# Kernel optimization log

Hardware: AMD Instinct MI355X
Metric: run time of the kernel (lower is better)

The kernel has to match this reference:

```python
import jax, jax.numpy as jnp
import numpy as np

K = 10
NUM_BLKS = 6
LN_EPS = 1e-6
NODE_D = 64


def layer_norm(x, g, b):
    m = jnp.mean(x, axis=-1, keepdims=True)
    v = jnp.var(x, axis=-1, keepdims=True)
    return (x - m) * jax.lax.rsqrt(v + LN_EPS) * g + b


def setup_inputs() -> dict:
    key = jax.random.key(0)
    B, N_c, N_t, D_S, D_F = 4, 4096, 1024, 3, 4
    D_IN = 4 + D_S + D_F  # obs-embed(4) + s + f
    ks = jax.random.split(key, 32)
    sc = 0.02
    inp = {
        "s_ctx": jax.random.normal(ks[0], (B, N_c, D_S), jnp.float32),
        "f_ctx": jax.random.normal(ks[1], (B, N_c, D_F), jnp.float32),
        "s_test": jax.random.normal(ks[2], (B, N_t, D_S), jnp.float32),
        "valid_lens_ctx": jax.random.randint(ks[3], (B,), N_c // 2, N_c + 1).astype(jnp.int32),
        # embed_obs: nn.Embed(2, 4)
        "emb_obs": jax.random.normal(ks[4], (2, 4), jnp.float32) * sc,
        # embed_all: MLP([256,128,64], gelu)
        "ea_W0": jax.random.normal(ks[5], (D_IN, 256), jnp.float32) * sc, "ea_b0": jnp.zeros((256,), jnp.float32),
        "ea_W1": jax.random.normal(ks[6], (256, 128), jnp.float32) * sc, "ea_b1": jnp.zeros((128,), jnp.float32),
        "ea_W2": jax.random.normal(ks[7], (128, NODE_D), jnp.float32) * sc, "ea_b2": jnp.zeros((NODE_D,), jnp.float32),
        # top-level LayerNorm
        "ln_g": jnp.ones((NODE_D,), jnp.float32), "ln_b": jnp.zeros((NODE_D,), jnp.float32),
        # GraphKRBlock params, stacked over NUM_BLKS blocks
        "blk_Wm0": jax.random.normal(ks[8], (NUM_BLKS, NODE_D + 1, 128), jnp.float32) * sc,
        "blk_bm0": jnp.zeros((NUM_BLKS, 128), jnp.float32),
        "blk_Wm1": jax.random.normal(ks[9], (NUM_BLKS, 128, NODE_D), jnp.float32) * sc,
        "blk_bm1": jnp.zeros((NUM_BLKS, NODE_D), jnp.float32),
        "blk_Wu0": jax.random.normal(ks[10], (NUM_BLKS, 2 * NODE_D, 128), jnp.float32) * sc,
        "blk_bu0": jnp.zeros((NUM_BLKS, 128), jnp.float32),
        "blk_Wu1": jax.random.normal(ks[11], (NUM_BLKS, 128, NODE_D), jnp.float32) * sc,
        "blk_bu1": jnp.zeros((NUM_BLKS, NODE_D), jnp.float32),
        "blk_lng": jnp.ones((NUM_BLKS, NODE_D), jnp.float32),
        "blk_lnb": jnp.zeros((NUM_BLKS, NODE_D), jnp.float32),
        # head: MLP([256,64,2], gelu)
        "hd_W0": jax.random.normal(ks[12], (NODE_D, 256), jnp.float32) * sc, "hd_b0": jnp.zeros((256,), jnp.float32),
        "hd_W1": jax.random.normal(ks[13], (256, 64), jnp.float32) * sc, "hd_b1": jnp.zeros((64,), jnp.float32),
        "hd_W2": jax.random.normal(ks[14], (64, 2), jnp.float32) * sc, "hd_b2": jnp.zeros((2,), jnp.float32),
    }
    return inp


def reference(s_ctx, f_ctx, s_test, valid_lens_ctx,
              emb_obs, ea_W0, ea_b0, ea_W1, ea_b1, ea_W2, ea_b2, ln_g, ln_b,
              blk_Wm0, blk_bm0, blk_Wm1, blk_bm1, blk_Wu0, blk_bu0, blk_Wu1, blk_bu1,
              blk_lng, blk_lnb, hd_W0, hd_b0, hd_W1, hd_b1, hd_W2, hd_b2):
    B, N_c, _ = s_ctx.shape
    N_t = s_test.shape[1]

    # --- per-sample O(n^2) KNN graph build (custom_k_nearest_senders, l2 dist) ---
    mask = jnp.arange(N_c)[None, :] < valid_lens_ctx[:, None]          # [B,N_c]
    s_send = jnp.where(mask[..., None], s_ctx, 1e6)                    # invalid -> far away
    rx = jnp.concatenate([s_ctx, s_test], axis=1)                      # [B,N,d_s] receivers
    d = jnp.sqrt(jnp.sum((rx[:, :, None, :] - s_send[:, None, :, :]) ** 2, axis=-1))  # [B,N,N_c]
    negd, senders = jax.lax.top_k(-d, K)                               # k-nearest: [B,N,K]
    dists = -negd                                                       # ascending distances

    # --- embeddings: stack(embed_obs, s, f) -> embed_all MLP -> LayerNorm ---
    def embed(x):
        h = jax.nn.gelu(x @ ea_W0 + ea_b0)
        h = jax.nn.gelu(h @ ea_W1 + ea_b1)
        h = h @ ea_W2 + ea_b2
        return layer_norm(h, ln_g, ln_b)

    ctx_in = jnp.concatenate(
        [jnp.broadcast_to(emb_obs[1], (B, N_c, emb_obs.shape[1])), s_ctx, f_ctx], axis=-1)
    test_in = jnp.concatenate(
        [jnp.broadcast_to(emb_obs[0], (B, N_t, emb_obs.shape[1])), s_test,
         jnp.zeros((B, N_t, f_ctx.shape[-1]), f_ctx.dtype)], axis=-1)
    nodes = jnp.concatenate([embed(ctx_in), embed(test_in)], axis=1)   # [B,N,64]

    # --- num_blks GraphKRBlock message-passing blocks ---
    bidx = jnp.arange(B)[:, None, None]
    w = jax.nn.softmax(-dists, axis=-1)                                # kernel weights per receiver
    for i in range(NUM_BLKS):
        sf = nodes[bidx, senders]                                      # gather senders [B,N,K,64]
        m_in = jnp.concatenate([sf, dists[..., None]], axis=-1)        # [B,N,K,65]
        m = jax.nn.gelu(m_in @ blk_Wm0[i] + blk_bm0[i]) @ blk_Wm1[i] + blk_bm1[i]
        agg = jnp.einsum('bnk,bnkd->bnd', w, m)                        # scatter-to-receivers
        u_in = jnp.concatenate([nodes, agg], axis=-1)                  # [B,N,128]
        upd = jax.nn.gelu(u_in @ blk_Wu0[i] + blk_bu0[i]) @ blk_Wu1[i] + blk_bu1[i]
        nodes = layer_norm(nodes + upd, blk_lng[i], blk_lnb[i])

    # --- head on test nodes ---
    x_t = nodes[:, N_c:, :]                                            # [B,N_t,64]
    h = jax.nn.gelu(x_t @ hd_W0 + hd_b0)
    h = jax.nn.gelu(h @ hd_W1 + hd_b1)
    f_dist = h @ hd_W2 + hd_b2                                         # [B,N_t,2]
    f_mu, f_log_var = jnp.split(f_dist, 2, axis=-1)
    f_std = jnp.exp(f_log_var / 2)                                     # min_std = 0.0
    return f_mu, f_std
```

## Files before the change

kernel.cpp:

```cpp
#include <hip/hip_runtime.h>
#include <math.h>

#define BB 4
#define NC 4096
#define NT 1024
#define NN (NC + NT)
#define NODES (BB * NN)
#define DD 64
#define KNN 10
#define NBLK 6
#define BIGF 3.0e38f

typedef __attribute__((ext_vector_type(8))) short short8;
typedef __attribute__((ext_vector_type(4))) float f32x4;
typedef __attribute__((ext_vector_type(4))) int int4v;

__device__ __forceinline__ unsigned short f2bf(float f) {
    unsigned int u = __float_as_uint(f);
    unsigned int r = (u + 0x7fffu + ((u >> 16) & 1u)) >> 16;
    return (unsigned short)r;
}
__device__ __forceinline__ float bf2f(unsigned short h) {
    return __uint_as_float(((unsigned int)h) << 16);
}

__device__ __forceinline__ float gelu_f(float x) {
    const float c0 = 0.7978845608028654f;
    float x3 = x * x * x;
    float z2 = 2.0f * c0 * (x + 0.044715f * x3);
    float e = __expf(z2);
    float r = __builtin_amdgcn_rcpf(1.0f + e);
    return x - x * r;
}

__device__ __forceinline__ float wave_sum(float v) {
#pragma unroll
    for (int off = 32; off > 0; off >>= 1) v += __shfl_xor(v, off, 64);
    return v;
}

__device__ __forceinline__ f32x4 mfma_bf16(short8 a, short8 b, f32x4 c) {
    asm("v_mfma_f32_16x16x32_bf16 %0, %1, %2, %0" : "+v"(c) : "v"(a), "v"(b));
    return c;
}


__global__ __launch_bounds__(256) void k_convw(
    const float* __restrict__ Wm0, const float* __restrict__ Wm1,
    const float* __restrict__ Wu0, const float* __restrict__ Wu1,
    const float* __restrict__ bm0,
    const float* __restrict__ eW0, const float* __restrict__ eW1,
    const float* __restrict__ eW2,
    const float* __restrict__ hW0, const float* __restrict__ hW1,
    const float* __restrict__ sctx, const int* __restrict__ valid_lens,
    unsigned short* __restrict__ wtm0, unsigned short* __restrict__ wtm1p,
    unsigned short* __restrict__ wtu0, unsigned short* __restrict__ wtu1,
    float* __restrict__ wdp, float* __restrict__ bm0p,
    unsigned short* __restrict__ wte0, unsigned short* __restrict__ wte1,
    unsigned short* __restrict__ wte2,
    unsigned short* __restrict__ wth0, unsigned short* __restrict__ wth1,
    float4* __restrict__ s4)
{
    int t = blockIdx.x * 256 + threadIdx.x;
    if (t < 49152) {
        int i = t / 8192, r = t % 8192, n = r / 64, k = r % 64;
        wtm0[t] = f2bf(Wm0[(i * 65 + k) * 128 + n]);
    } else if (t < 98304) {
        int u = t - 49152;
        int i = u / 8192, r = u % 8192, n = r / 128, cp = r % 128;
        int col = ((cp & 7) << 4) | (cp >> 3);
        wtm1p[u] = f2bf(Wm1[(i * 128 + col) * 64 + n]);
    } else if (t < 196608) {
        int u = t - 98304;
        int i = u / 16384, r = u % 16384, n = r / 128, k = r % 128;
        wtu0[u] = f2bf(Wu0[(i * 128 + k) * 128 + n]);
    } else if (t < 245760) {
        int u = t - 196608;
        int i = u / 8192, r = u % 8192, n = r / 128, k = r % 128;
        wtu1[u] = f2bf(Wu1[(i * 128 + k) * 64 + n]);
    } else if (t < 246528) {
        int u = t - 245760;
        int i = u / 128, cp = u % 128;
        int col = ((cp & 7) << 4) | (cp >> 3);
        wdp[u] = Wm0[(i * 65 + 64) * 128 + col];
    } else if (t < 247296) {
        int u = t - 246528;
        int i = u / 128, cp = u % 128;
        int col = ((cp & 7) << 4) | (cp >> 3);
        bm0p[u] = bm0[i * 128 + col];
    } else if (t < 255488) {
        int u = t - 247296;
        int n = u / 32, k = u % 32;
        wte0[u] = (k < 11) ? f2bf(eW0[k * 256 + n]) : 0;
    } else if (t < 288256) {
        int u = t - 255488;
        int n = u / 256, k = u % 256;
        wte1[u] = f2bf(eW1[k * 128 + n]);
    } else if (t < 296448) {
        int u = t - 288256;
        int n = u / 128, k = u % 128;
        wte2[u] = f2bf(eW2[k * 64 + n]);
    } else if (t < 312832) {
        int u = t - 296448;
        int n = u / 64, k = u % 64;
        wth0[u] = f2bf(hW0[k * 256 + n]);
    } else if (t < 329216) {
        int u = t - 312832;
        int n = u / 256, k = u % 256;
        wth1[u] = f2bf(hW1[k * 64 + n]);
    } else if (t < 329216 + BB * NC) {
        int u = t - 329216;
        int b = u / NC, j = u % NC;
        bool ok = j < valid_lens[b];
        float x = ok ? sctx[u * 3] : 1.0e6f;
        float y = ok ? sctx[u * 3 + 1] : 1.0e6f;
        float z = ok ? sctx[u * 3 + 2] : 1.0e6f;
        s4[u] = make_float4(x, y, z, 0.0f);
    }
}

__global__ __launch_bounds__(256) void k_embed2(
    const float* __restrict__ s_ctx, const float* __restrict__ f_ctx,
    const float* __restrict__ s_test, const float* __restrict__ emb_obs,
    const unsigned short* __restrict__ WT0, const float* __restrict__ b0,
    const unsigned short* __restrict__ WT1, const float* __restrict__ b1,
    const unsigned short* __restrict__ WT2, const float* __restrict__ b2,
    const float* __restrict__ g, const float* __restrict__ bta,
    const unsigned short* __restrict__ Wm0n,
    unsigned short* __restrict__ nodes,
    unsigned short* __restrict__ Pout)
{
    __shared__ unsigned short H0[4][16 * 256];
    __shared__ unsigned short H1[4][16 * 128];
    __shared__ unsigned short XO[4][16 * 64];
    int t = threadIdx.x;
    int wave = t >> 6, lane = t & 63, lr = lane & 15, lk = lane >> 4;
    int rb = wave * 16;
    int n0 = blockIdx.x * 64;
    int bq = n0 / NN, nloc0 = n0 % NN;
    bool is_ctx = nloc0 < NC;
    int nr = nloc0 + rb + lr;
    float xv[8];
#pragma unroll
    for (int j = 0; j < 8; ++j) xv[j] = 0.0f;
    if (lk == 0) {
        const float* eb = emb_obs + (is_ctx ? 4 : 0);
        xv[0] = eb[0]; xv[1] = eb[1]; xv[2] = eb[2]; xv[3] = eb[3];
        if (is_ctx) {
            const float* sp = s_ctx + ((size_t)(bq * NC + nr)) * 3;
            const float* fp = f_ctx + ((size_t)(bq * NC + nr)) * 4;
            xv[4] = sp[0]; xv[5] = sp[1]; xv[6] = sp[2]; xv[7] = fp[0];
        } else {
            const float* sp = s_test + ((size_t)(bq * NT + nr - NC)) * 3;
            xv[4] = sp[0]; xv[5] = sp[1]; xv[6] = sp[2];
        }
    } else if (lk == 1 && is_ctx) {
        const float* fp = f_ctx + ((size_t)(bq * NC + nr)) * 4;
        xv[0] = fp[1]; xv[1] = fp[2]; xv[2] = fp[3];
    }
    short8 a;
#pragma unroll
    for (int j = 0; j < 8; ++j) a[j] = (short)f2bf(xv[j]);

    f32x4 acc0[16];
#pragma unroll
    for (int nt = 0; nt < 16; ++nt) {
        short8 bb = *(const short8*)(WT0 + (nt * 16 + lr) * 32 + lk * 8);
        f32x4 z = (f32x4){0.f, 0.f, 0.f, 0.f};
        acc0[nt] = mfma_bf16(a, bb, z);
    }
    unsigned short* h0 = &H0[wave][0];
#pragma unroll
    for (int nt = 0; nt < 16; ++nt) {
        int col = nt * 16 + lr;
        float bias = b0[col];
        int u = col >> 3;
#pragma unroll
        for (int j = 0; j < 4; ++j) {
            int row = lk * 4 + j;
            float v = gelu_f(acc0[nt][j] + bias);
            int us = (u & 16) | ((u ^ row) & 15);
            h0[row * 256 + us * 8 + (col & 7)] = f2bf(v);
        }
    }
    f32x4 acc1[8];
#pragma unroll
    for (int nt = 0; nt < 8; ++nt) acc1[nt] = (f32x4){0.f, 0.f, 0.f, 0.f};
#pragma unroll
    for (int ks = 0; ks < 8; ++ks) {
        int u = ks * 4 + lk;
        int us = (u & 16) | ((u ^ lr) & 15);
        short8 aa = *(const short8*)(&h0[lr * 256 + us * 8]);
#pragma unroll
        for (int nt = 0; nt < 8; ++nt) {
            short8 bb = *(const short8*)(WT1 + (nt * 16 + lr) * 256 + ks * 32 + lk * 8);
            acc1[nt] = mfma_bf16(aa, bb, acc1[nt]);
        }
    }
    unsigned short* h1 = &H1[wave][0];
#pragma unroll
    for (int nt = 0; nt < 8; ++nt) {
        int col = nt * 16 + lr;
        float bias = b1[col];
        int u = col >> 3;
#pragma unroll
        for (int j = 0; j < 4; ++j) {
            int row = lk * 4 + j;
            float v = gelu_f(acc1[nt][j] + bias);
            int us = (u ^ row) & 15;
            h1[row * 128 + us * 8 + (col & 7)] = f2bf(v);
        }
    }
    f32x4 acc2[4];
#pragma unroll
    for (int nt = 0; nt < 4; ++nt) acc2[nt] = (f32x4){0.f, 0.f, 0.f, 0.f};
#pragma unroll
    for (int ks = 0; ks < 4; ++ks) {
        int u = ks * 4 + lk;
        int us = (u ^ lr) & 15;
        short8 aa = *(const short8*)(&h1[lr * 128 + us * 8]);
#pragma unroll
        for (int nt = 0; nt < 4; ++nt) {
            short8 bb = *(const short8*)(WT2 + (nt * 16 + lr) * 128 + ks * 32 + lk * 8);
            acc2[nt] = mfma_bf16(aa, bb, acc2[nt]);
        }
    }
    float vals[4][4];
#pragma unroll
    for (int j = 0; j < 4; ++j)
#pragma unroll
        for (int nt = 0; nt < 4; ++nt)
            vals[j][nt] = acc2[nt][j] + b2[nt * 16 + lr];
    unsigned short* xo = &XO[wave][0];
#pragma unroll
    for (int j = 0; j < 4; ++j) {
        float s = vals[j][0] + vals[j][1] + vals[j][2] + vals[j][3];
#pragma unroll
        for (int m = 1; m < 16; m <<= 1) s += __shfl_xor(s, m, 64);
        float mean = s * (1.0f / 64.0f);
        float vs = 0.0f;
#pragma unroll
        for (int nt = 0; nt < 4; ++nt) { float d = vals[j][nt] - mean; vs += d * d; }
#pragma unroll
        for (int m = 1; m < 16; m <<= 1) vs += __shfl_xor(vs, m, 64);
        float inv = rsqrtf(vs * (1.0f / 64.0f) + 1e-6f);
        int row = lk * 4 + j;
        int node = n0 + rb + row;
#pragma unroll
        for (int nt = 0; nt < 4; ++nt) {
            int col = nt * 16 + lr;
            float o = (vals[j][nt] - mean) * inv * g[col] + bta[col];
            unsigned short ob = f2bf(o);
            nodes[(size_t)node * 64 + col] = ob;
            xo[row * 64 + ((col >> 3) ^ (row & 7)) * 8 + (col & 7)] = ob;
        }
    }
    f32x4 accP[8];
#pragma unroll
    for (int nt = 0; nt < 8; ++nt) accP[nt] = (f32x4){0.f, 0.f, 0.f, 0.f};
#pragma unroll
    for (int ks = 0; ks < 2; ++ks) {
        short8 aa = *(const short8*)(&xo[lr * 64 + ((ks * 4 + lk) ^ (lr & 7)) * 8]);
#pragma unroll
        for (int nt = 0; nt < 8; ++nt) {
            short8 bb = *(const short8*)(Wm0n + (nt * 16 + lr) * 64 + ks * 32 + lk * 8);
            accP[nt] = mfma_bf16(aa, bb, accP[nt]);
        }
    }
#pragma unroll
    for (int j = 0; j < 4; ++j) {
        int node = n0 + rb + lk * 4 + j;
        short8 ps;
#pragma unroll
        for (int nt = 0; nt < 8; ++nt) ps[nt] = (short)f2bf(accP[nt][j]);
        *(short8*)(Pout + (size_t)node * 128 + lr * 8) = ps;
    }
}

__global__ __launch_bounds__(256) void k_topk(
    const float4* __restrict__ s4, const float* __restrict__ s_ctx,
    const float* __restrict__ s_test,
    float* __restrict__ dists, int* __restrict__ senders, float* __restrict__ wout)
{
    __shared__ float cd[4 * 64 * 11];
    __shared__ float seld[4][4][12];
    __shared__ int   seli[4][4][12];
    __shared__ int   eqis[4][4][12];
    int wave = threadIdx.x >> 6;
    int lane = threadIdx.x & 63;
    int r0 = blockIdx.x * 16 + wave * 4;
    int b = r0 / NN;
    const float4* sc = s4 + (size_t)b * NC;
    float px[4], py[4], pz[4];
#pragma unroll
    for (int q = 0; q < 4; ++q) {
        int n = (r0 + q) % NN;
        const float* p = (n < NC) ? &s_ctx[(size_t)(b * NC + n) * 3]
                                  : &s_test[(size_t)(b * NT + (n - NC)) * 3];
        px[q] = p[0]; py[q] = p[1]; pz[q] = p[2];
    }
    float bq[4][KNN];
#pragma unroll
    for (int q = 0; q < 4; ++q)
#pragma unroll
        for (int k = 0; k < KNN; ++k) bq[q][k] = BIGF;
#pragma unroll 8
    for (int i = 0; i < 64; ++i) {
        int j = lane + (i << 6);
        float4 s = sc[j];
#pragma unroll
        for (int q = 0; q < 4; ++q) {
            float dx = px[q] - s.x, dy = py[q] - s.y, dz = pz[q] - s.z;
            float d2 = fmaf(dx, dx, fmaf(dy, dy, dz * dz));
#pragma unroll
            for (int k = KNN - 1; k >= 1; --k)
                bq[q][k] = __builtin_amdgcn_fmed3f(bq[q][k - 1], bq[q][k], d2);
            bq[q][0] = fminf(bq[q][0], d2);
        }
    }
    int base = (wave * 64 + lane) * 11;
    float T[4], dmin[4];
    int m[4];
#pragma unroll
    for (int q = 0; q < 4; ++q) {
#pragma unroll
        for (int k = 0; k < KNN; ++k) cd[base + k] = bq[q][k];
        __builtin_amdgcn_wave_barrier();
        int head = 0;
        float myd = 0.0f;
#pragma unroll
        for (int rr = 0; rr < KNN; ++rr) {
            float v = cd[base + head];
            float mv = v;
#pragma unroll
            for (int off = 32; off > 0; off >>= 1) mv = fminf(mv, __shfl_xor(mv, off, 64));
            unsigned long long ball = __ballot(v == mv);
            int win = __ffsll(ball) - 1;
            if (lane == win) head++;
            if (lane == rr) myd = mv;
        }
        T[q] = __shfl(myd, 9, 64);
        dmin[q] = sqrtf(__shfl(myd, 0, 64));
        m[q] = __popcll(__ballot(lane < KNN && myd < T[q]));
    }
    unsigned long long below = (lane == 63) ? 0x7FFFFFFFFFFFFFFFull
                                            : ((1ull << lane) - 1);
    int cless[4] = {0, 0, 0, 0}, ceq[4] = {0, 0, 0, 0};
#pragma unroll 4
    for (int i = 0; i < 64; ++i) {
        int j = lane + (i << 6);
        float4 s = sc[j];
#pragma unroll
        for (int q = 0; q < 4; ++q) {
            float dx = px[q] - s.x, dy = py[q] - s.y, dz = pz[q] - s.z;
            float v = fmaf(dx, dx, fmaf(dy, dy, dz * dz));
            unsigned long long ml = __ballot(v < T[q]);
            unsigned long long me = __ballot(v == T[q]);
            if (v < T[q]) {
                int slot = cless[q] + __popcll(ml & below);
                if (slot < 12) { seld[wave][q][slot] = v; seli[wave][q][slot] = j; }
            }
            if (v == T[q]) {
                int qq = ceq[q] + __popcll(me & below);
                if (qq < 12) eqis[wave][q][qq] = j;
            }
            cless[q] += __popcll(ml);
            ceq[q] += __popcll(me);
        }
    }
    __builtin_amdgcn_wave_barrier();
#pragma unroll
    for (int q = 0; q < 4; ++q) {
        float e = 0.0f, d = 0.0f;
        int isel = 0;
        if (lane < KNN) {
            float vsel;
            if (lane < m[q]) { vsel = seld[wave][q][lane]; isel = seli[wave][q][lane]; }
            else             { vsel = T[q];                isel = eqis[wave][q][lane - m[q]]; }
            d = sqrtf(vsel);
            e = __expf(-(d - dmin[q]));
        }
        float ssum = wave_sum(e);
        if (lane < KNN) {
            size_t o = (size_t)(r0 + q) * KNN + lane;
            dists[o] = d;
            senders[o] = isel;
            wout[o] = e / ssum;
        }
    }
}

__global__ __launch_bounds__(256) void k_blk(
    const unsigned short* __restrict__ nodes_in,
    const unsigned short* __restrict__ P,
    const float* __restrict__ dists, const int* __restrict__ senders,
    const float* __restrict__ w,
    const float* __restrict__ wdp, const float* __restrict__ bm0p,
    const unsigned short* __restrict__ Wm1p,
    const float* __restrict__ bm1,
    const unsigned short* __restrict__ WTu0,
    const float* __restrict__ bu0,
    const unsigned short* __restrict__ WTu1,
    const float* __restrict__ bu1,
    const float* __restrict__ lng, const float* __restrict__ lnb,
    const unsigned short* __restrict__ Wm0n,
    const int doP,
    unsigned short* __restrict__ nodes_out,
    unsigned short* __restrict__ Pout,
    const int doHead,
    const unsigned short* __restrict__ wth0,
    const float* __restrict__ hb0,
    const unsigned short* __restrict__ wth1,
    const float* __restrict__ hb1,
    const float* __restrict__ hW2, const float* __restrict__ hb2,
    float* __restrict__ out)
{
    __shared__ unsigned short X[16 * 64];
    __shared__ unsigned short G[16 * 128];
    __shared__ unsigned short AG[16 * 64];
    __shared__ unsigned short H[16 * 128];
    __shared__ unsigned short XO[16 * 64];
    __shared__ unsigned short HH[16 * 256];
    __shared__ unsigned short HH1[16 * 72];
    __shared__ int   sidE[160];
    __shared__ float dE[160], wE[160];
    int l = threadIdx.x;
    int wave = l >> 6, lane = l & 63;
    int n0 = blockIdx.x * 16;
    int b = n0 / NN;
    size_t bbase = (size_t)b * NN;
    int e0 = n0 * KNN;
    if (l < 160) {
        sidE[l] = senders[e0 + l];
        dE[l]   = dists[e0 + l];
        wE[l]   = w[e0 + l];
    }
    if (l < 128) {
        int row = l >> 3, u = l & 7;
        int4v v = *(const int4v*)(nodes_in + ((size_t)(n0 + row)) * 64 + u * 8);
        *(int4v*)(&X[row * 64 + (u ^ (row & 7)) * 8]) = v;
    }
    __syncthreads();
    float wd0 = wdp[2 * lane], wd1 = wdp[2 * lane + 1];
    float bb0 = bm0p[2 * lane], bb1 = bm0p[2 * lane + 1];
    const unsigned int* Pb = (const unsigned int*)P;
    unsigned int* G32 = (unsigned int*)G;
#pragma unroll
    for (int nn = 0; nn < 4; ++nn) {
        int n = wave * 4 + nn;
        float a0 = 0.0f, a1 = 0.0f;
#pragma unroll
        for (int k = 0; k < KNN; ++k) {
            int e = n * KNN + k;
            int sid = sidE[e];
            float dd = dE[e], ww = wE[e];
            unsigned int pr = Pb[(bbase + sid) * 64 + lane];
            float p0 = __uint_as_float(pr << 16);
            float p1 = __uint_as_float(pr & 0xFFFF0000u);
            float g0 = gelu_f(fmaf(dd, wd0, p0 + bb0));
            float g1 = gelu_f(fmaf(dd, wd1, p1 + bb1));
            a0 = fmaf(ww, g0, a0);
            a1 = fmaf(ww, g1, a1);
        }
        unsigned int pk = (unsigned int)f2bf(a0) | ((unsigned int)f2bf(a1) << 16);
        G32[n * 64 + ((lane >> 2) ^ n) * 4 + (lane & 3)] = pk;
    }
    __syncthreads();
    if (wave != 0) return;
    int lr = lane & 15, lk = lane >> 4;
    f32x4 accA[4];
#pragma unroll
    for (int nt = 0; nt < 4; ++nt) accA[nt] = (f32x4){0.f, 0.f, 0.f, 0.f};
#pragma unroll
    for (int ks = 0; ks < 4; ++ks) {
        short8 a = *(const short8*)(&G[lr * 128 + ((ks * 4 + lk) ^ lr) * 8]);
#pragma unroll
        for (int nt = 0; nt < 4; ++nt) {
            short8 bb = *(const short8*)(Wm1p + (nt * 16 + lr) * 128 + ks * 32 + lk * 8);
            accA[nt] = mfma_bf16(a, bb, accA[nt]);
        }
    }
#pragma unroll
    for (int nt = 0; nt < 4; ++nt) {
        int col = nt * 16 + lr;
        float bias = bm1[col];
#pragma unroll
        for (int j = 0; j < 4; ++j) {
            int row = lk * 4 + j;
            AG[row * 64 + ((col >> 3) ^ (row & 7)) * 8 + (col & 7)] =
                f2bf(accA[nt][j] + bias);
        }
    }
    f32x4 acc[8];
#pragma unroll
    for (int nt = 0; nt < 8; ++nt) acc[nt] = (f32x4){0.f, 0.f, 0.f, 0.f};
#pragma unroll
    for (int ks = 0; ks < 4; ++ks) {
        short8 a;
        if (ks < 2) a = *(const short8*)(&X[lr * 64 + ((ks * 4 + lk) ^ (lr & 7)) * 8]);
        else        a = *(const short8*)(&AG[lr * 64 + (((ks - 2) * 4 + lk) ^ (lr & 7)) * 8]);
#pragma unroll
        for (int nt = 0; nt < 8; ++nt) {
            short8 bb = *(const short8*)(WTu0 + (nt * 16 + lr) * 128 + ks * 32 + lk * 8);
            acc[nt] = mfma_bf16(a, bb, acc[nt]);
        }
    }
#pragma unroll
    for (int nt = 0; nt < 8; ++nt) {
        int col = nt * 16 + lr;
        float bias = bu0[col];
#pragma unroll
        for (int j = 0; j < 4; ++j) {
            int lrow = lk * 4 + j;
            float v = gelu_f(acc[nt][j] + bias);
            H[lrow * 128 + ((col >> 3) ^ lrow) * 8 + (col & 7)] = f2bf(v);
        }
    }
    f32x4 acc2[4];
#pragma unroll
    for (int nt = 0; nt < 4; ++nt) acc2[nt] = (f32x4){0.f, 0.f, 0.f, 0.f};
#pragma unroll
    for (int ks = 0; ks < 4; ++ks) {
        short8 a = *(const short8*)(&H[lr * 128 + ((ks * 4 + lk) ^ lr) * 8]);
#pragma unroll
        for (int nt = 0; nt < 4; ++nt) {
            short8 bb = *(const short8*)(WTu1 + (nt * 16 + lr) * 128 + ks * 32 + lk * 8);
            acc2[nt] = mfma_bf16(a, bb, acc2[nt]);
        }
    }
    float vals[4][4];
#pragma unroll
    for (int j = 0; j < 4; ++j) {
        int row = lk * 4 + j;
#pragma unroll
        for (int nt = 0; nt < 4; ++nt) {
            int col = nt * 16 + lr;
            float x = bf2f(X[row * 64 + ((col >> 3) ^ (row & 7)) * 8 + (col & 7)]);
            vals[j][nt] = x + acc2[nt][j] + bu1[col];
        }
    }
#pragma unroll
    for (int j = 0; j < 4; ++j) {
        int row = lk * 4 + j;
        float s = vals[j][0] + vals[j][1] + vals[j][2] + vals[j][3];
#pragma unroll
        for (int mm = 1; mm < 16; mm <<= 1) s += __shfl_xor(s, mm, 64);
        float mean = s * (1.0f / 64.0f);
        float vs = 0.0f;
#pragma unroll
        for (int nt = 0; nt < 4; ++nt) { float d = vals[j][nt] - mean; vs += d * d; }
#pragma unroll
        for (int mm = 1; mm < 16; mm <<= 1) vs += __shfl_xor(vs, mm, 64);
        float inv = rsqrtf(vs * (1.0f / 64.0f) + 1e-6f);
#pragma unroll
        for (int nt = 0; nt < 4; ++nt) {
            int col = nt * 16 + lr;
            float o = (vals[j][nt] - mean) * inv * lng[col] + lnb[col];
            unsigned short ob = f2bf(o);
            nodes_out[((size_t)(n0 + row)) * 64 + col] = ob;
            XO[row * 64 + ((col >> 3) ^ (row & 7)) * 8 + (col & 7)] = ob;
        }
    }
    if (doP) {
        f32x4 accP[8];
#pragma unroll
        for (int nt = 0; nt < 8; ++nt) accP[nt] = (f32x4){0.f, 0.f, 0.f, 0.f};
#pragma unroll
        for (int ks = 0; ks < 2; ++ks) {
            short8 aa = *(const short8*)(&XO[lr * 64 + ((ks * 4 + lk) ^ (lr & 7)) * 8]);
#pragma unroll
            for (int nt = 0; nt < 8; ++nt) {
                short8 bb = *(const short8*)(Wm0n + (nt * 16 + lr) * 64 + ks * 32 + lk * 8);
                accP[nt] = mfma_bf16(aa, bb, accP[nt]);
            }
        }
#pragma unroll
        for (int j = 0; j < 4; ++j) {
            int node = n0 + lk * 4 + j;
            short8 ps;
#pragma unroll
            for (int nt = 0; nt < 8; ++nt) ps[nt] = (short)f2bf(accP[nt][j]);
            *(short8*)(Pout + (size_t)node * 128 + lr * 8) = ps;
        }
    }
    int nloc = n0 % NN;
    if (doHead && nloc >= NC) {
        int bq = n0 / NN;
#pragma unroll
        for (int half = 0; half < 2; ++half) {
            f32x4 ah[8];
#pragma unroll
            for (int nt = 0; nt < 8; ++nt) ah[nt] = (f32x4){0.f, 0.f, 0.f, 0.f};
#pragma unroll
            for (int ks = 0; ks < 2; ++ks) {
                short8 aa = *(const short8*)(&XO[lr * 64 + ((ks * 4 + lk) ^ (lr & 7)) * 8]);
#pragma unroll
                for (int nt = 0; nt < 8; ++nt) {
                    int col16 = half * 8 + nt;
                    short8 bb = *(const short8*)(wth0 + (col16 * 16 + lr) * 64 + ks * 32 + lk * 8);
                    ah[nt] = mfma_bf16(aa, bb, ah[nt]);
                }
            }
#pragma unroll
            for (int nt = 0; nt < 8; ++nt) {
                int col = (half * 8 + nt) * 16 + lr;
                float bias = hb0[col];
                int u = col >> 3;
#pragma unroll
                for (int j = 0; j < 4; ++j) {
                    int row = lk * 4 + j;
                    float v = gelu_f(ah[nt][j] + bias);
                    int us = (u & 16) | ((u ^ row) & 15);
                    HH[row * 256 + us * 8 + (col & 7)] = f2bf(v);
                }
            }
        }
        f32x4 a1h[4];
#pragma unroll
        for (int nt = 0; nt < 4; ++nt) a1h[nt] = (f32x4){0.f, 0.f, 0.f, 0.f};
#pragma unroll
        for (int ks = 0; ks < 8; ++ks) {
            int u = ks * 4 + lk;
            int us = (u & 16) | ((u ^ lr) & 15);
            short8 aa = *(const short8*)(&HH[lr * 256 + us * 8]);
#pragma unroll
            for (int nt = 0; nt < 4; ++nt) {
                short8 bb = *(const short8*)(wth1 + (nt * 16 + lr) * 256 + ks * 32 + lk * 8);
                a1h[nt] = mfma_bf16(aa, bb, a1h[nt]);
            }
        }
#pragma unroll
        for (int nt = 0; nt < 4; ++nt) {
            int col = nt * 16 + lr;
            float bias = hb1[col];
#pragma unroll
            for (int j = 0; j < 4; ++j) {
                int row = lk * 4 + j;
                HH1[row * 72 + col] = f2bf(gelu_f(a1h[nt][j] + bias));
            }
        }
        int task = lane >> 1;
        int row = task >> 1;
        int o = task & 1;
        int t2 = lane & 1;
        float pp = 0.0f;
#pragma unroll
        for (int d = 0; d < 32; ++d) {
            int dd = t2 * 32 + d;
            pp += bf2f(HH1[row * 72 + dd]) * hW2[dd * 2 + o];
        }
        pp += __shfl_xor(pp, 1, 64);
        if (t2 == 0) {
            int gg = bq * NT + (nloc - NC) + row;
            if (o == 0) out[gg] = pp + hb2[0];
            else        out[BB * NT + gg] = __expf(0.5f * (pp + hb2[1]));
        }
    }
}

extern "C" void kernel_launch(void* const* d_in, const int* in_sizes, int n_in,
                              void* d_out, int out_size, void* d_ws, size_t ws_size,
                              hipStream_t stream)
{
    (void)in_sizes; (void)n_in; (void)out_size; (void)ws_size;
    const float* s_ctx   = (const float*)d_in[0];
    const float* f_ctx   = (const float*)d_in[1];
    const float* s_test  = (const float*)d_in[2];
    const int*   valid   = (const int*)d_in[3];
    const float* emb_obs = (const float*)d_in[4];
    const float* ea_W0   = (const float*)d_in[5];
    const float* ea_b0   = (const float*)d_in[6];
    const float* ea_W1   = (const float*)d_in[7];
    const float* ea_b1   = (const float*)d_in[8];
    const float* ea_W2   = (const float*)d_in[9];
    const float* ea_b2   = (const float*)d_in[10];
    const float* ln_g    = (const float*)d_in[11];
    const float* ln_b    = (const float*)d_in[12];
    const float* blk_Wm0 = (const float*)d_in[13];
    const float* blk_bm0 = (const float*)d_in[14];
    const float* blk_Wm1 = (const float*)d_in[15];
    const float* blk_bm1 = (const float*)d_in[16];
    const float* blk_Wu0 = (const float*)d_in[17];
    const float* blk_bu0 = (const float*)d_in[18];
    const float* blk_Wu1 = (const float*)d_in[19];
    const float* blk_bu1 = (const float*)d_in[20];
    const float* blk_lng = (const float*)d_in[21];
    const float* blk_lnb = (const float*)d_in[22];
    const float* hd_W0   = (const float*)d_in[23];
    const float* hd_b0   = (const float*)d_in[24];
    const float* hd_W1   = (const float*)d_in[25];
    const float* hd_b1   = (const float*)d_in[26];
    const float* hd_W2   = (const float*)d_in[27];
    const float* hd_b2   = (const float*)d_in[28];

    char* p = (char*)d_ws;
    auto alloc = [&](size_t bytes) { char* r = p; p += (bytes + 255) & ~(size_t)255; return r; };
    unsigned short* nodesA = (unsigned short*)alloc((size_t)NODES * 64 * 2);
    unsigned short* nodesB = (unsigned short*)alloc((size_t)NODES * 64 * 2);
    unsigned short* PA     = (unsigned short*)alloc((size_t)NODES * 128 * 2);
    unsigned short* PB     = (unsigned short*)alloc((size_t)NODES * 128 * 2);
    float* dists   = (float*)alloc((size_t)NODES * KNN * 4);
    float* wbuf    = (float*)alloc((size_t)NODES * KNN * 4);
    int*   senders = (int*)alloc((size_t)NODES * KNN * 4);
    unsigned short* wtm0  = (unsigned short*)alloc((size_t)6 * 8192 * 2);
    unsigned short* wtm1p = (unsigned short*)alloc((size_t)6 * 8192 * 2);
    unsigned short* wtu0  = (unsigned short*)alloc((size_t)6 * 16384 * 2);
    unsigned short* wtu1  = (unsigned short*)alloc((size_t)6 * 8192 * 2);
    float* wdp  = (float*)alloc((size_t)6 * 128 * 4);
    float* bm0p = (float*)alloc((size_t)6 * 128 * 4);
    unsigned short* wte0 = (unsigned short*)alloc((size_t)8192 * 2);
    unsigned short* wte1 = (unsigned short*)alloc((size_t)32768 * 2);
    unsigned short* wte2 = (unsigned short*)alloc((size_t)8192 * 2);
    unsigned short* wth0 = (unsigned short*)alloc((size_t)16384 * 2);
    unsigned short* wth1 = (unsigned short*)alloc((size_t)16384 * 2);
    float4* s4 = (float4*)alloc((size_t)BB * NC * 16);

    k_convw<<<1350, 256, 0, stream>>>(
        blk_Wm0, blk_Wm1, blk_Wu0, blk_Wu1, blk_bm0,
        ea_W0, ea_W1, ea_W2, hd_W0, hd_W1, s_ctx, valid,
        wtm0, wtm1p, wtu0, wtu1, wdp, bm0p, wte0, wte1, wte2, wth0, wth1, s4);

    k_embed2<<<NODES / 64, 256, 0, stream>>>(s_ctx, f_ctx, s_test, emb_obs,
        wte0, ea_b0, wte1, ea_b1, wte2, ea_b2, ln_g, ln_b, wtm0, nodesA, PA);

    k_topk<<<NODES / 16, 256, 0, stream>>>(s4, s_ctx, s_test,
                                           dists, senders, wbuf);

    unsigned short* nin = nodesA; unsigned short* nout = nodesB;
    unsigned short* pin = PA;     unsigned short* pout = PB;
    for (int i = 0; i < NBLK; ++i) {
        int doP = (i < NBLK - 1) ? 1 : 0;
        int doHead = (i == NBLK - 1) ? 1 : 0;
        const unsigned short* wm0n = wtm0 + (size_t)((i + 1) % NBLK) * 8192;
        k_blk<<<NODES / 16, 256, 0, stream>>>(nin, pin, dists, senders, wbuf,
            wdp + (size_t)i * 128, bm0p + (size_t)i * 128,
            wtm1p + (size_t)i * 8192, blk_bm1 + (size_t)i * 64,
            wtu0 + (size_t)i * 16384, blk_bu0 + (size_t)i * 128,
            wtu1 + (size_t)i * 8192, blk_bu1 + (size_t)i * 64,
            blk_lng + (size_t)i * 64, blk_lnb + (size_t)i * 64,
            wm0n, doP, nout, pout,
            doHead, wth0, hd_b0, wth1, hd_b1, hd_W2, hd_b2, (float*)d_out);
        unsigned short* tmp = nin; nin = nout; nout = tmp;
        tmp = pin; pin = pout; pout = tmp;
    }
}
```

Baseline: 304.5 us.

## Skip context nodes in last block, expand-distance top-k, split P projection wave

The last graph block now launches only over test-node tiles, since only test nodes feed the head, and skips context-node work there. The top-k search ranks candidates by the expanded form |s|^2 - 2p·s, with |s|^2 precomputed into the padding lane of s4. True distances are recomputed only for the ten selected neighbours, and the softmax drops the dmin shift. The block kernel moves the next-block P projection onto wave 1 after a barrier, and tile order is interleaved across blocks. The expanded distance can change tie-breaking and neighbour selection through rounding, and the unshifted exp risks underflow when distances are large.

```diff
diff --git a/kernel.cpp b/kernel.cpp
--- a/kernel.cpp
+++ b/kernel.cpp
@@ -115,7 +115,8 @@
         float x = ok ? sctx[u * 3] : 1.0e6f;
         float y = ok ? sctx[u * 3 + 1] : 1.0e6f;
         float z = ok ? sctx[u * 3 + 2] : 1.0e6f;
-        s4[u] = make_float4(x, y, z, 0.0f);
+        float w2 = fmaf(x, x, fmaf(y, y, z * z));
+        s4[u] = make_float4(x, y, z, w2);
     }
 }
 
@@ -283,7 +284,6 @@
     float* __restrict__ dists, int* __restrict__ senders, float* __restrict__ wout)
 {
     __shared__ float cd[4 * 64 * 11];
-    __shared__ float seld[4][4][12];
     __shared__ int   seli[4][4][12];
     __shared__ int   eqis[4][4][12];
     int wave = threadIdx.x >> 6;
@@ -291,13 +291,14 @@
     int r0 = blockIdx.x * 16 + wave * 4;
     int b = r0 / NN;
     const float4* sc = s4 + (size_t)b * NC;
-    float px[4], py[4], pz[4];
+    float px[4], py[4], pz[4], m2x[4], m2y[4], m2z[4];
 #pragma unroll
     for (int q = 0; q < 4; ++q) {
         int n = (r0 + q) % NN;
         const float* p = (n < NC) ? &s_ctx[(size_t)(b * NC + n) * 3]
                                   : &s_test[(size_t)(b * NT + (n - NC)) * 3];
         px[q] = p[0]; py[q] = p[1]; pz[q] = p[2];
+        m2x[q] = -2.0f * px[q]; m2y[q] = -2.0f * py[q]; m2z[q] = -2.0f * pz[q];
     }
     float bq[4][KNN];
 #pragma unroll
@@ -310,16 +311,15 @@
         float4 s = sc[j];
 #pragma unroll
         for (int q = 0; q < 4; ++q) {
-            float dx = px[q] - s.x, dy = py[q] - s.y, dz = pz[q] - s.z;
-            float d2 = fmaf(dx, dx, fmaf(dy, dy, dz * dz));
+            float v = fmaf(s.x, m2x[q], fmaf(s.y, m2y[q], fmaf(s.z, m2z[q], s.w)));
 #pragma unroll
             for (int k = KNN - 1; k >= 1; --k)
-                bq[q][k] = __builtin_amdgcn_fmed3f(bq[q][k - 1], bq[q][k], d2);
-            bq[q][0] = fminf(bq[q][0], d2);
+                bq[q][k] = __builtin_amdgcn_fmed3f(bq[q][k - 1], bq[q][k], v);
+            bq[q][0] = fminf(bq[q][0], v);
         }
     }
     int base = (wave * 64 + lane) * 11;
-    float T[4], dmin[4];
+    float T[4];
     int m[4];
 #pragma unroll
     for (int q = 0; q < 4; ++q) {
@@ -340,7 +340,6 @@
             if (lane == rr) myd = mv;
         }
         T[q] = __shfl(myd, 9, 64);
-        dmin[q] = sqrtf(__shfl(myd, 0, 64));
         m[q] = __popcll(__ballot(lane < KNN && myd < T[q]));
     }
     unsigned long long below = (lane == 63) ? 0x7FFFFFFFFFFFFFFFull
@@ -352,13 +351,12 @@
         float4 s = sc[j];
 #pragma unroll
         for (int q = 0; q < 4; ++q) {
-            float dx = px[q] - s.x, dy = py[q] - s.y, dz = pz[q] - s.z;
-            float v = fmaf(dx, dx, fmaf(dy, dy, dz * dz));
+            float v = fmaf(s.x, m2x[q], fmaf(s.y, m2y[q], fmaf(s.z, m2z[q], s.w)));
             unsigned long long ml = __ballot(v < T[q]);
             unsigned long long me = __ballot(v == T[q]);
             if (v < T[q]) {
                 int slot = cless[q] + __popcll(ml & below);
-                if (slot < 12) { seld[wave][q][slot] = v; seli[wave][q][slot] = j; }
+                if (slot < 12) seli[wave][q][slot] = j;
             }
             if (v == T[q]) {
                 int qq = ceq[q] + __popcll(me & below);
@@ -374,11 +372,11 @@
         float e = 0.0f, d = 0.0f;
         int isel = 0;
         if (lane < KNN) {
-            float vsel;
-            if (lane < m[q]) { vsel = seld[wave][q][lane]; isel = seli[wave][q][lane]; }
-            else             { vsel = T[q];                isel = eqis[wave][q][lane - m[q]]; }
-            d = sqrtf(vsel);
-            e = __expf(-(d - dmin[q]));
+            isel = (lane < m[q]) ? seli[wave][q][lane] : eqis[wave][q][lane - m[q]];
+            float4 s = sc[isel];
+            float dx = px[q] - s.x, dy = py[q] - s.y, dz = pz[q] - s.z;
+            d = sqrtf(fmaf(dx, dx, fmaf(dy, dy, dz * dz)));
+            e = __expf(-d);
         }
         float ssum = wave_sum(e);
         if (lane < KNN) {
@@ -407,7 +405,7 @@
     const int doP,
     unsigned short* __restrict__ nodes_out,
     unsigned short* __restrict__ Pout,
-    const int doHead,
+    const int doHead, const int testOnly,
     const unsigned short* __restrict__ wth0,
     const float* __restrict__ hb0,
     const unsigned short* __restrict__ wth1,
@@ -426,7 +424,10 @@
     __shared__ float dE[160], wE[160];
     int l = threadIdx.x;
     int wave = l >> 6, lane = l & 63;
-    int n0 = blockIdx.x * 16;
+    int bid = blockIdx.x;
+    int tile = testOnly ? ((bid >> 6) * 320 + 256 + (bid & 63))
+                        : ((bid & 7) * 160 + (bid >> 3));
+    int n0 = tile * 16;
     int b = n0 / NN;
     size_t bbase = (size_t)b * NN;
     int e0 = n0 * KNN;
@@ -466,102 +467,104 @@
         G32[n * 64 + ((lane >> 2) ^ n) * 4 + (lane & 3)] = pk;
     }
     __syncthreads();
-    if (wave != 0) return;
     int lr = lane & 15, lk = lane >> 4;
-    f32x4 accA[4];
-#pragma unroll
-    for (int nt = 0; nt < 4; ++nt) accA[nt] = (f32x4){0.f, 0.f, 0.f, 0.f};
-#pragma unroll
-    for (int ks = 0; ks < 4; ++ks) {
-        short8 a = *(const short8*)(&G[lr * 128 + ((ks * 4 + lk) ^ lr) * 8]);
+    if (wave == 0) {
+        f32x4 accA[4];
+#pragma unroll
+        for (int nt = 0; nt < 4; ++nt) accA[nt] = (f32x4){0.f, 0.f, 0.f, 0.f};
+#pragma unroll
+        for (int ks = 0; ks < 4; ++ks) {
+            short8 a = *(const short8*)(&G[lr * 128 + ((ks * 4 + lk) ^ lr) * 8]);
+#pragma unroll
+            for (int nt = 0; nt < 4; ++nt) {
+                short8 bb = *(const short8*)(Wm1p + (nt * 16 + lr) * 128 + ks * 32 + lk * 8);
+                accA[nt] = mfma_bf16(a, bb, accA[nt]);
+            }
+        }
 #pragma unroll
         for (int nt = 0; nt < 4; ++nt) {
-            short8 bb = *(const short8*)(Wm1p + (nt * 16 + lr) * 128 + ks * 32 + lk * 8);
-            accA[nt] = mfma_bf16(a, bb, accA[nt]);
-        }
-    }
-#pragma unroll
-    for (int nt = 0; nt < 4; ++nt) {
-        int col = nt * 16 + lr;
-        float bias = bm1[col];
+            int col = nt * 16 + lr;
+            float bias = bm1[col];
+#pragma unroll
+            for (int j = 0; j < 4; ++j) {
+                int row = lk * 4 + j;
+                AG[row * 64 + ((col >> 3) ^ (row & 7)) * 8 + (col & 7)] =
+                    f2bf(accA[nt][j] + bias);
+            }
+        }
+        f32x4 acc[8];
+#pragma unroll
+        for (int nt = 0; nt < 8; ++nt) acc[nt] = (f32x4){0.f, 0.f, 0.f, 0.f};
+#pragma unroll
+        for (int ks = 0; ks < 4; ++ks) {
+            short8 a;
+            if (ks < 2) a = *(const short8*)(&X[lr * 64 + ((ks * 4 + lk) ^ (lr & 7)) * 8]);
+            else        a = *(const short8*)(&AG[lr * 64 + (((ks - 2) * 4 + lk) ^ (lr & 7)) * 8]);
+#pragma unroll
+            for (int nt = 0; nt < 8; ++nt) {
+                short8 bb = *(const short8*)(WTu0 + (nt * 16 + lr) * 128 + ks * 32 + lk * 8);
+                acc[nt] = mfma_bf16(a, bb, acc[nt]);
+            }
+        }
+#pragma unroll
+        for (int nt = 0; nt < 8; ++nt) {
+            int col = nt * 16 + lr;
+            float bias = bu0[col];
+#pragma unroll
+            for (int j = 0; j < 4; ++j) {
+                int lrow = lk * 4 + j;
+                float v = gelu_f(acc[nt][j] + bias);
+                H[lrow * 128 + ((col >> 3) ^ lrow) * 8 + (col & 7)] = f2bf(v);
+            }
+        }
+        f32x4 acc2[4];
+#pragma unroll
+        for (int nt = 0; nt < 4; ++nt) acc2[nt] = (f32x4){0.f, 0.f, 0.f, 0.f};
+#pragma unroll
+        for (int ks = 0; ks < 4; ++ks) {
+            short8 a = *(const short8*)(&H[lr * 128 + ((ks * 4 + lk) ^ lr) * 8]);
+#pragma unroll
+            for (int nt = 0; nt < 4; ++nt) {
+                short8 bb = *(const short8*)(WTu1 + (nt * 16 + lr) * 128 + ks * 32 + lk * 8);
+                acc2[nt] = mfma_bf16(a, bb, acc2[nt]);
+            }
+        }
+        float vals[4][4];
 #pragma unroll
         for (int j = 0; j < 4; ++j) {
             int row = lk * 4 + j;
-            AG[row * 64 + ((col >> 3) ^ (row & 7)) * 8 + (col & 7)] =
-                f2bf(accA[nt][j] + bias);
-        }
-    }
-    f32x4 acc[8];
-#pragma unroll
-    for (int nt = 0; nt < 8; ++nt) acc[nt] = (f32x4){0.f, 0.f, 0.f, 0.f};
-#pragma unroll
-    for (int ks = 0; ks < 4; ++ks) {
-        short8 a;
-        if (ks < 2) a = *(const short8*)(&X[lr * 64 + ((ks * 4 + lk) ^ (lr & 7)) * 8]);
-        else        a = *(const short8*)(&AG[lr * 64 + (((ks - 2) * 4 + lk) ^ (lr & 7)) * 8]);
-#pragma unroll
-        for (int nt = 0; nt < 8; ++nt) {
-            short8 bb = *(const short8*)(WTu0 + (nt * 16 + lr) * 128 + ks * 32 + lk * 8);
-            acc[nt] = mfma_bf16(a, bb, acc[nt]);
-        }
-    }
-#pragma unroll
-    for (int nt = 0; nt < 8; ++nt) {
-        int col = nt * 16 + lr;
-        float bias = bu0[col];
+#pragma unroll
+            for (int nt = 0; nt < 4; ++nt) {
+                int col = nt * 16 + lr;
+                float x = bf2f(X[row * 64 + ((col >> 3) ^ (row & 7)) * 8 + (col & 7)]);
+                vals[j][nt] = x + acc2[nt][j] + bu1[col];
+            }
+        }
 #pragma unroll
         for (int j = 0; j < 4; ++j) {
-            int lrow = lk * 4 + j;
-            float v = gelu_f(acc[nt][j] + bias);
-            H[lrow * 128 + ((col >> 3) ^ lrow) * 8 + (col & 7)] = f2bf(v);
-        }
-    }
-    f32x4 acc2[4];
-#pragma unroll
-    for (int nt = 0; nt < 4; ++nt) acc2[nt] = (f32x4){0.f, 0.f, 0.f, 0.f};
-#pragma unroll
-    for (int ks = 0; ks < 4; ++ks) {
-        short8 a = *(const short8*)(&H[lr * 128 + ((ks * 4 + lk) ^ lr) * 8]);
-#pragma unroll
-        for (int nt = 0; nt < 4; ++nt) {
-            short8 bb = *(const short8*)(WTu1 + (nt * 16 + lr) * 128 + ks * 32 + lk * 8);
-            acc2[nt] = mfma_bf16(a, bb, acc2[nt]);
-        }
-    }
-    float vals[4][4];
-#pragma unroll
-    for (int j = 0; j < 4; ++j) {
-        int row = lk * 4 + j;
-#pragma unroll
-        for (int nt = 0; nt < 4; ++nt) {
-            int col = nt * 16 + lr;
-            float x = bf2f(X[row * 64 + ((col >> 3) ^ (row & 7)) * 8 + (col & 7)]);
-            vals[j][nt] = x + acc2[nt][j] + bu1[col];
-        }
-    }
-#pragma unroll
-    for (int j = 0; j < 4; ++j) {
-        int row = lk * 4 + j;
-        float s = vals[j][0] + vals[j][1] + vals[j][2] + vals[j][3];
-#pragma unroll
-        for (int mm = 1; mm < 16; mm <<= 1) s += __shfl_xor(s, mm, 64);
-        float mean = s * (1.0f / 64.0f);
-        float vs = 0.0f;
-#pragma unroll
-        for (int nt = 0; nt < 4; ++nt) { float d = vals[j][nt] - mean; vs += d * d; }
-#pragma unroll
-        for (int mm = 1; mm < 16; mm <<= 1) vs += __shfl_xor(vs, mm, 64);
-        float inv = rsqrtf(vs * (1.0f / 64.0f) + 1e-6f);
-#pragma unroll
-        for (int nt = 0; nt < 4; ++nt) {
-            int col = nt * 16 + lr;
-            float o = (vals[j][nt] - mean) * inv * lng[col] + lnb[col];
-            unsigned short ob = f2bf(o);
-            nodes_out[((size_t)(n0 + row)) * 64 + col] = ob;
-            XO[row * 64 + ((col >> 3) ^ (row & 7)) * 8 + (col & 7)] = ob;
-        }
-    }
-    if (doP) {
+            int row = lk * 4 + j;
+            float s = vals[j][0] + vals[j][1] + vals[j][2] + vals[j][3];
+#pragma unroll
+            for (int mm = 1; mm < 16; mm <<= 1) s += __shfl_xor(s, mm, 64);
+            float mean = s * (1.0f / 64.0f);
+            float vs = 0.0f;
+#pragma unroll
+            for (int nt = 0; nt < 4; ++nt) { float d = vals[j][nt] - mean; vs += d * d; }
+#pragma unroll
+            for (int mm = 1; mm < 16; mm <<= 1) vs += __shfl_xor(vs, mm, 64);
+            float inv = rsqrtf(vs * (1.0f / 64.0f) + 1e-6f);
+#pragma unroll
+            for (int nt = 0; nt < 4; ++nt) {
+                int col = nt * 16 + lr;
+                float o = (vals[j][nt] - mean) * inv * lng[col] + lnb[col];
+                unsigned short ob = f2bf(o);
+                nodes_out[((size_t)(n0 + row)) * 64 + col] = ob;
+                XO[row * 64 + ((col >> 3) ^ (row & 7)) * 8 + (col & 7)] = ob;
+            }
+        }
+    }
+    __syncthreads();
+    if (doP && wave == 1) {
         f32x4 accP[8];
 #pragma unroll
         for (int nt = 0; nt < 8; ++nt) accP[nt] = (f32x4){0.f, 0.f, 0.f, 0.f};
@@ -583,8 +586,8 @@
             *(short8*)(Pout + (size_t)node * 128 + lr * 8) = ps;
         }
     }
-    int nloc = n0 % NN;
-    if (doHead && nloc >= NC) {
+    if (doHead && wave == 0) {
+        int nloc = n0 % NN;
         int bq = n0 / NN;
 #pragma unroll
         for (int half = 0; half < 2; ++half) {
@@ -731,15 +734,17 @@
     for (int i = 0; i < NBLK; ++i) {
         int doP = (i < NBLK - 1) ? 1 : 0;
         int doHead = (i == NBLK - 1) ? 1 : 0;
+        int testOnly = doHead;
+        int grid = testOnly ? (BB * NT / 16) : (NODES / 16);
         const unsigned short* wm0n = wtm0 + (size_t)((i + 1) % NBLK) * 8192;
-        k_blk<<<NODES / 16, 256, 0, stream>>>(nin, pin, dists, senders, wbuf,
+        k_blk<<<grid, 256, 0, stream>>>(nin, pin, dists, senders, wbuf,
             wdp + (size_t)i * 128, bm0p + (size_t)i * 128,
             wtm1p + (size_t)i * 8192, blk_bm1 + (size_t)i * 64,
             wtu0 + (size_t)i * 16384, blk_bu0 + (size_t)i * 128,
             wtu1 + (size_t)i * 8192, blk_bu1 + (size_t)i * 64,
             blk_lng + (size_t)i * 64, blk_lnb + (size_t)i * 64,
             wm0n, doP, nout, pout,
-            doHead, wth0, hd_b0, wth1, hd_b1, hd_W2, hd_b2, (float*)d_out);
+            doHead, testOnly, wth0, hd_b0, wth1, hd_b1, hd_W2, hd_b2, (float*)d_out);
         unsigned short* tmp = nin; nin = nout; nout = tmp;
         tmp = pin; pin = pout; pout = tmp;
     }
```

Measured after the change: 325.4 us. 1.07x slower.
